# Kernel tuning notes

Hardware: AMD Instinct MI355X
Metric: run time of the kernel (lower is better)

The kernel has to match this reference:

```python
import jax, jax.numpy as jnp
import numpy as np

B, L, D = 32, 256, 128


def hard_sigmoid(x):
    # Keras-1 default inner_activation for LSTM gates
    return jnp.clip(0.2 * x + 0.5, 0.0, 1.0)


def lstm_step(x_t, h, c, W, U, b):
    # Keras-1 gate order: i, f, c(candidate), o
    z = x_t @ W + h @ U + b  # [B, 4D]
    d = h.shape[-1]
    i = hard_sigmoid(z[:, :d])
    f = hard_sigmoid(z[:, d:2 * d])
    g = jnp.tanh(z[:, 2 * d:3 * d])
    o = hard_sigmoid(z[:, 3 * d:])
    c_new = f * c + i * g
    h_new = o * jnp.tanh(c_new)
    return h_new, c_new


def setup_inputs() -> dict:
    key = jax.random.key(0)
    ks = jax.random.split(key, 9)
    s = 0.05  # weight scale to keep activations in a sane range
    return {
        "x": jax.random.normal(ks[0], (B, L, D), dtype=jnp.float32),
        "Wr": jax.random.normal(ks[1], (D, 4 * D), dtype=jnp.float32) * s,
        "Ur": jax.random.normal(ks[2], (D, 4 * D), dtype=jnp.float32) * s,
        "br": jnp.zeros((4 * D,), dtype=jnp.float32),
        "Ww": jax.random.normal(ks[3], (D, 4 * D), dtype=jnp.float32) * s,
        "Uw": jax.random.normal(ks[4], (D, 4 * D), dtype=jnp.float32) * s,
        "bw": jnp.zeros((4 * D,), dtype=jnp.float32),
        "Wc": jax.random.normal(ks[5], (2 * D, D), dtype=jnp.float32) * s,
        "bc": jnp.zeros((D,), dtype=jnp.float32),
    }


def reference(x, Wr, Ur, br, Ww, Uw, bw, Wc, bc):
    b, l, d = x.shape
    h0 = jnp.zeros((b, d), dtype=x.dtype)

    # ---- reader LSTM (return_sequences) ----
    def reader_step(carry, x_t):
        h, c = carry
        h, c = lstm_step(x_t, h, c, Wr, Ur, br)
        return (h, c), h

    _, o_seq = jax.lax.scan(reader_step, (h0, h0), jnp.swapaxes(x, 0, 1))  # [L, B, D]

    # ---- compose-and-write scan over timesteps ----
    mem0 = x  # read() sets mem_0 = input

    def write_step(carry, o_t):
        mem, h, c = carry  # mem: [B, L, D]
        # eq 2-3: attention over memory slots
        z = jax.nn.softmax(jnp.einsum('bd,bld->bl', o_t, mem), axis=-1)  # [B, L]
        m_rt = jnp.einsum('bl,bld->bd', z, mem)  # [B, D]
        # eq 4: composer (linear activation)
        c_t = jnp.concatenate([o_t, m_rt], axis=-1) @ Wc + bc  # [B, D]
        # eq 5: writer LSTM step
        h, c = lstm_step(c_t, h, c, Ww, Uw, bw)
        # eq 6: soft overwrite of memory
        zc = z[:, :, None]
        mem = mem * (1.0 - zc) + h[:, None, :] * zc
        return (mem, h, c), h

    (_, _, _), hs = jax.lax.scan(write_step, (mem0, h0, h0), o_seq)
    # return_mode == 'last_output'
    return hs[-1]
```

## Files before the change

kernel.cpp:

```cpp
#include <hip/hip_runtime.h>
#include <stdint.h>


#define LL 256

typedef float v2f __attribute__((ext_vector_type(2)));

__device__ __forceinline__ float hsig(float x) { return fminf(fmaxf(fmaf(x, 0.2f, 0.5f), 0.f), 1.f); }
__device__ __forceinline__ float tanh_fast(float x) {
  x = fminf(fmaxf(x, -15.f), 15.f);
  float e = __expf(2.f * x);
  return (e - 1.f) / (e + 1.f);
}

__global__ __launch_bounds__(512) void wtrans_kernel(const float* __restrict__ src,
                                                     float* __restrict__ dst, int jshift) {
  int idx = blockIdx.x * 512 + threadIdx.x;
  int J = 1 << jshift;
  int k = idx >> jshift, j = idx & (J - 1);
  dst[(((size_t)(k >> 2) << jshift) + j) * 4 + (k & 3)] = src[idx];
}

__global__ __launch_bounds__(512) void pvw_gemm(const float* __restrict__ Wc,
                                                const float* __restrict__ Ww,
                                                float* __restrict__ PVw) {
  __shared__ float wrow[128];
  const int r = blockIdx.x, j = threadIdx.x;
  if (j < 128) wrow[j] = Wc[r * 128 + j];
  __syncthreads();
  float a = 0.f;
#pragma unroll 4
  for (int m = 0; m < 128; m++) a = fmaf(wrow[m], Ww[m * 512 + j], a);
  PVw[r * 512 + j] = a;
}

__global__ __launch_bounds__(512) void pz_kernel(const float* __restrict__ bc,
                                                 const float* __restrict__ Ww,
                                                 const float* __restrict__ bw,
                                                 float* __restrict__ pz) {
  __shared__ float b_s[128];
  const int j = threadIdx.x;
  if (j < 128) b_s[j] = bc[j];
  __syncthreads();
  float a = bw[j];
#pragma unroll 4
  for (int m = 0; m < 128; m++) a = fmaf(b_s[m], Ww[m * 512 + j], a);
  pz[j] = a;
}

__global__ __launch_bounds__(512) void xw_gemm(const float* __restrict__ x,
                                               const float4* __restrict__ WrT4,
                                               const float* __restrict__ br,
                                               float* __restrict__ XW) {
  alignas(16) __shared__ float xs[8][128];
  const int b = blockIdx.x >> 5, tg = blockIdx.x & 31, tid = threadIdx.x;
  const float* xg = x + ((size_t)b * LL + tg * 8) * 128;
  if (tid < 256) ((float4*)&xs[0][0])[tid] = ((const float4*)xg)[tid];
  __syncthreads();
  float acc[8];
#pragma unroll
  for (int r = 0; r < 8; r++) acc[r] = 0.f;
#pragma unroll 8
  for (int i4 = 0; i4 < 32; i4++) {
    float4 w4 = WrT4[i4 * 512 + tid];
#pragma unroll
    for (int r = 0; r < 8; r++) {
      float4 v = *(const float4*)&xs[r][4 * i4];
      acc[r] += w4.x * v.x + w4.y * v.y + w4.z * v.z + w4.w * v.w;
    }
  }
  const float brj = br[tid];
  float* o = XW + ((size_t)b * LL + tg * 8) * 512;
#pragma unroll
  for (int r = 0; r < 8; r++) o[r * 512 + tid] = acc[r] + brj;
}

__global__ __launch_bounds__(512, 2) void reader_kernel(const float4* __restrict__ UrT4,
                                                        const float* __restrict__ XW,
                                                        float* __restrict__ og) {
  alignas(16) __shared__ float h_s[128];
  alignas(16) __shared__ float pp_s[512];
  const int b = blockIdx.x, tid = threadIdx.x;
  const float* XWb = XW + (size_t)b * LL * 512;
  float* ogb = og + (size_t)b * LL * 128;

  float4 U[32];
#pragma unroll
  for (int i4 = 0; i4 < 32; i4++) U[i4] = UrT4[i4 * 512 + tid];

  float c_r = 0.f;
  if (tid < 128) h_s[tid] = 0.f;
  float xwv = XWb[tid];
  __syncthreads();

  for (int t = 0; t < LL; t++) {
    float xw_n = (t + 1 < LL) ? XWb[(t + 1) * 512 + tid] : 0.f;
    v2f acc[4] = {{0.f, 0.f}, {0.f, 0.f}, {0.f, 0.f}, {0.f, 0.f}};
#pragma unroll
    for (int i4 = 0; i4 < 32; i4++) {
      float4 v = *(const float4*)&h_s[4 * i4];
      float4 w = U[i4];
      acc[i4 & 3] += (v2f){w.x, w.y} * (v2f){v.x, v.y};
      acc[i4 & 3] += (v2f){w.z, w.w} * (v2f){v.z, v.w};
    }
    v2f A = (acc[0] + acc[1]) + (acc[2] + acc[3]);
    pp_s[tid] = A.x + A.y + xwv;
    __syncthreads();
    if (tid < 128) {
      float zi = pp_s[tid], zf = pp_s[128 + tid], zg = pp_s[256 + tid], zo = pp_s[384 + tid];
      float ii = hsig(zi), ff = hsig(zf), gg = tanh_fast(zg), oo = hsig(zo);
      c_r = fmaf(ff, c_r, ii * gg);
      float h = oo * tanh_fast(c_r);
      h_s[tid] = h;
      ogb[t * 128 + tid] = h;
    }
    __syncthreads();
    xwv = xw_n;
  }
}

template <int NC>
__global__ __launch_bounds__(512, 2) void writer_kernel(
    const float* __restrict__ x,
    const float4* __restrict__ VwT4, const float4* __restrict__ UwT4,
    const float* __restrict__ og, const float* __restrict__ ZW,
    float* __restrict__ out) {
  alignas(16) __shared__ float h_s[128];
  alignas(16) __shared__ float osN[128];
  alignas(16) __shared__ float sc_s[256], ee_s[256];
  alignas(16) __shared__ float mr_s[128];
  alignas(16) __shared__ float pp_s[1024];
  __shared__ float rr_s[16];
  extern __shared__ float4 UwL[];

  const int b = blockIdx.x, tid = threadIdx.x;
  const int lane = tid & 63, wv = tid >> 6;
  const int l = tid >> 1, hf = tid & 1;
  const int q = tid >> 6, dp = tid & 63;

  const float* xg = x + (size_t)b * (LL * 128);
  const float* ogb = og + (size_t)b * (LL * 128);
  const float* ZWb = ZW + (size_t)b * (LL * 512);

  for (int i = tid; i < NC * 512; i += 512) UwL[i] = UwT4[i];

  float4 VR[16];
#pragma unroll
  for (int i4 = 0; i4 < 16; i4++) VR[i4] = VwT4[i4 * 512 + tid];

  v2f Mr[32], Mc[32];
#pragma unroll
  for (int w = 0; w < 32; w++) Mr[w] = *(const v2f*)(xg + l * 128 + hf * 64 + 2 * w);
#pragma unroll
  for (int i = 0; i < 32; i++) Mc[i] = *(const v2f*)(xg + (q * 32 + i) * 128 + 2 * dp);

  float c_w = 0.f;
  if (tid < 128) { h_s[tid] = 0.f; osN[tid] = ogb[tid]; }
  __syncthreads();
  {
    v2f S = {0.f, 0.f};
#pragma unroll
    for (int w = 0; w < 32; w++) S += Mr[w] * (*(const v2f*)&osN[hf * 64 + 2 * w]);
    float s = S.x + S.y;
    s += __shfl_xor(s, 1);
    if (hf == 0) sc_s[l] = s;
  }
  __syncthreads();

  for (int t = 0; t < LL; t++) {
    float huv;
    {
      float zwv = ZWb[(size_t)t * 512 + tid];
      v2f u0 = {0.f, 0.f}, u1 = {0.f, 0.f};
#pragma unroll 2
      for (int i4 = NC; i4 < 32; i4 += 2) {
        float4 w0 = UwT4[i4 * 512 + tid];
        float4 w1 = UwT4[(i4 + 1) * 512 + tid];
        float4 v0 = *(const float4*)&h_s[4 * i4];
        float4 v1 = *(const float4*)&h_s[4 * i4 + 4];
        u0 += (v2f){w0.x, w0.y} * (v2f){v0.x, v0.y};
        u0 += (v2f){w0.z, w0.w} * (v2f){v0.z, v0.w};
        u1 += (v2f){w1.x, w1.y} * (v2f){v1.x, v1.y};
        u1 += (v2f){w1.z, w1.w} * (v2f){v1.z, v1.w};
      }
#pragma unroll 2
      for (int i4 = 0; i4 < NC; i4 += 2) {
        float4 w0 = UwL[i4 * 512 + tid];
        float4 w1 = UwL[(i4 + 1) * 512 + tid];
        float4 v0 = *(const float4*)&h_s[4 * i4];
        float4 v1 = *(const float4*)&h_s[4 * i4 + 4];
        u0 += (v2f){w0.x, w0.y} * (v2f){v0.x, v0.y};
        u0 += (v2f){w0.z, w0.w} * (v2f){v0.z, v0.w};
        u1 += (v2f){w1.x, w1.y} * (v2f){v1.x, v1.y};
        u1 += (v2f){w1.z, w1.w} * (v2f){v1.z, v1.w};
      }
      v2f U = u0 + u1;
      huv = U.x + U.y + zwv;
    }
    if (tid >= 128 && tid < 256 && t + 1 < LL)
      osN[tid - 128] = ogb[(t + 1) * 128 + (tid - 128)];
    if (tid < 256) {
      float m = sc_s[tid];
#pragma unroll
      for (int off = 32; off > 0; off >>= 1) m = fmaxf(m, __shfl_xor(m, off));
      if (lane == 0) rr_s[wv] = m;
    }
    __syncthreads();
    if (tid < 256) {
      float mx = fmaxf(fmaxf(rr_s[0], rr_s[1]), fmaxf(rr_s[2], rr_s[3]));
      float e = __expf(sc_s[tid] - mx);
      ee_s[tid] = e;
      float s2 = e;
#pragma unroll
      for (int off = 32; off > 0; off >>= 1) s2 += __shfl_xor(s2, off);
      if (lane == 0) rr_s[8 + wv] = s2;
    }
    __syncthreads();
    const float inv = 1.f / (rr_s[8] + rr_s[9] + rr_s[10] + rr_s[11]);
    {
      v2f P = {0.f, 0.f};
#pragma unroll
      for (int i = 0; i < 32; i++) P += Mc[i] * ee_s[q * 32 + i];
      *(v2f*)&pp_s[q * 128 + 2 * dp] = P;
    }
    __syncthreads();
    if (tid < 128) {
      float s = 0.f;
#pragma unroll
      for (int g = 0; g < 8; g++) s += pp_s[g * 128 + tid];
      mr_s[tid] = s * inv;
    }
    __syncthreads();
    {
      v2f a0 = {0.f, 0.f}, a1 = {0.f, 0.f}, a2 = {0.f, 0.f}, a3 = {0.f, 0.f};
#pragma unroll 2
      for (int i4 = 16; i4 < 32; i4 += 2) {
        float4 w0 = VwT4[i4 * 512 + tid];
        float4 w1 = VwT4[(i4 + 1) * 512 + tid];
        float4 v0 = *(const float4*)&mr_s[4 * i4];
        float4 v1 = *(const float4*)&mr_s[4 * i4 + 4];
        a0 += (v2f){w0.x, w0.y} * (v2f){v0.x, v0.y};
        a0 += (v2f){w0.z, w0.w} * (v2f){v0.z, v0.w};
        a1 += (v2f){w1.x, w1.y} * (v2f){v1.x, v1.y};
        a1 += (v2f){w1.z, w1.w} * (v2f){v1.z, v1.w};
      }
#pragma unroll
      for (int i4 = 0; i4 < 16; i4 += 2) {
        float4 w0 = VR[i4];
        float4 w1 = VR[i4 + 1];
        float4 v0 = *(const float4*)&mr_s[4 * i4];
        float4 v1 = *(const float4*)&mr_s[4 * i4 + 4];
        a2 += (v2f){w0.x, w0.y} * (v2f){v0.x, v0.y};
        a2 += (v2f){w0.z, w0.w} * (v2f){v0.z, v0.w};
        a3 += (v2f){w1.x, w1.y} * (v2f){v1.x, v1.y};
        a3 += (v2f){w1.z, w1.w} * (v2f){v1.z, v1.w};
      }
      v2f A = (a0 + a2) + (a1 + a3);
      pp_s[tid] = A.x + A.y + huv;
    }
    __syncthreads();
    if (tid < 128) {
      float zi = pp_s[tid], zf = pp_s[128 + tid], zg = pp_s[256 + tid], zo = pp_s[384 + tid];
      float ii = hsig(zi), ff = hsig(zf), gg = tanh_fast(zg), oo = hsig(zo);
      c_w = fmaf(ff, c_w, ii * gg);
      h_s[tid] = oo * tanh_fast(c_w);
    }
    __syncthreads();
    if (t + 1 < LL) {
      const float zr = ee_s[l] * inv;
      v2f S = {0.f, 0.f};
#pragma unroll
      for (int w = 0; w < 32; w++) {
        v2f h2 = *(const v2f*)&h_s[hf * 64 + 2 * w];
        v2f m = Mr[w];
        v2f n = m + (h2 - m) * zr;
        Mr[w] = n;
        S += n * (*(const v2f*)&osN[hf * 64 + 2 * w]);
      }
      float s = S.x + S.y;
      s += __shfl_xor(s, 1);
      if (hf == 0) sc_s[l] = s;
      v2f hc = *(const v2f*)&h_s[2 * dp];
#pragma unroll
      for (int i = 0; i < 32; i++) {
        float zc = ee_s[q * 32 + i] * inv;
        v2f m = Mc[i];
        Mc[i] = m + (hc - m) * zc;
      }
    }
    __syncthreads();
  }

  if (tid < 128) out[b * 128 + tid] = h_s[tid];
}

extern "C" void kernel_launch(void* const* d_in, const int* in_sizes, int n_in,
                              void* d_out, int out_size, void* d_ws, size_t ws_size,
                              hipStream_t stream) {
  const float* x  = (const float*)d_in[0];
  const float* Wr = (const float*)d_in[1];
  const float* Ur = (const float*)d_in[2];
  const float* br = (const float*)d_in[3];
  const float* Ww = (const float*)d_in[4];
  const float* Uw = (const float*)d_in[5];
  const float* bw = (const float*)d_in[6];
  const float* Wc = (const float*)d_in[7];
  const float* bc = (const float*)d_in[8];
  float* out = (float*)d_out;

  float* og  = (float*)d_ws;
  float* XW  = og + 1048576;
  float* WrT = XW + 4194304;
  float* UrT = WrT + 65536;
  float* UwT = UrT + 65536;
  float* PVw = UwT + 65536;
  float* PwT = PVw + 131072;
  float* VwT = PwT + 65536;
  float* pz  = VwT + 65536;

  static int nc_cached = -1;
  if (nc_cached < 0) {
    int want = 18 * 512 * (int)sizeof(float4);
    nc_cached = (hipFuncSetAttribute(
                     reinterpret_cast<const void*>(&writer_kernel<18>),
                     hipFuncAttributeMaxDynamicSharedMemorySize, want) == hipSuccess)
                    ? 18
                    : 6;
  }

  wtrans_kernel<<<128, 512, 0, stream>>>(Wr, WrT, 9);
  wtrans_kernel<<<128, 512, 0, stream>>>(Ur, UrT, 9);
  wtrans_kernel<<<128, 512, 0, stream>>>(Uw, UwT, 9);
  pvw_gemm<<<256, 512, 0, stream>>>(Wc, Ww, PVw);
  pz_kernel<<<1, 512, 0, stream>>>(bc, Ww, bw, pz);
  wtrans_kernel<<<128, 512, 0, stream>>>(PVw, PwT, 9);
  wtrans_kernel<<<128, 512, 0, stream>>>(PVw + 65536, VwT, 9);
  xw_gemm<<<1024, 512, 0, stream>>>(x, (const float4*)WrT, br, XW);
  reader_kernel<<<32, 512, 0, stream>>>((const float4*)UrT, XW, og);
  xw_gemm<<<1024, 512, 0, stream>>>(og, (const float4*)PwT, pz, XW);
  if (nc_cached == 18) {
    writer_kernel<18><<<32, 512, 18 * 512 * sizeof(float4), stream>>>(
        x, (const float4*)VwT, (const float4*)UwT, og, XW, out);
  } else {
    writer_kernel<6><<<32, 512, 6 * 512 * sizeof(float4), stream>>>(
        x, (const float4*)VwT, (const float4*)UwT, og, XW, out);
  }
}
```

Measured before the change: 1.880 ms.

## Merge softmax reductions into one barrier, hold Uw slice in registers, prefetch ZW

The two-barrier softmax becomes a single pass. Each wave computes its local max and exp-sum, and the four wave partials are combined afterwards with rescaling factors. The 1/sum normalisation is folded into the Vw matvec output and the memory-update weights. The register-resident weight slice moves from 16 float4 of Vw to up to 14 float4 of Uw plus 4 of Vw, and the next step's ZW row is prefetched one iteration ahead. The intent is to remove a barrier and hide global-load latency, at the cost of register pressure under launch_bounds(512,2), with possible spills.

```diff
diff --git a/kernel.cpp b/kernel.cpp
--- a/kernel.cpp
+++ b/kernel.cpp
@@ -125,6 +125,9 @@
     const float4* __restrict__ VwT4, const float4* __restrict__ UwT4,
     const float* __restrict__ og, const float* __restrict__ ZW,
     float* __restrict__ out) {
+  constexpr int UR_N = (32 - NC < 14) ? (32 - NC) : 14;
+  constexpr int STR_LO = NC, STR_HI = 32 - UR_N;
+
   alignas(16) __shared__ float h_s[128];
   alignas(16) __shared__ float osN[128];
   alignas(16) __shared__ float sc_s[256], ee_s[256];
@@ -144,9 +147,13 @@
 
   for (int i = tid; i < NC * 512; i += 512) UwL[i] = UwT4[i];
 
-  float4 VR[16];
-#pragma unroll
-  for (int i4 = 0; i4 < 16; i4++) VR[i4] = VwT4[i4 * 512 + tid];
+  float4 UR[UR_N];
+#pragma unroll
+  for (int r = 0; r < UR_N; r++) UR[r] = UwT4[(size_t)(STR_HI + r) * 512 + tid];
+
+  float4 VR[4];
+#pragma unroll
+  for (int r = 0; r < 4; r++) VR[r] = VwT4[(size_t)(28 + r) * 512 + tid];
 
   v2f Mr[32], Mc[32];
 #pragma unroll
@@ -167,60 +174,70 @@
   }
   __syncthreads();
 
+  float zwv = ZWb[tid];
   for (int t = 0; t < LL; t++) {
+    const int tn = (t + 1 < LL) ? t + 1 : t;
+    float zw_n = ZWb[(size_t)tn * 512 + tid];
+
     float huv;
     {
-      float zwv = ZWb[(size_t)t * 512 + tid];
-      v2f u0 = {0.f, 0.f}, u1 = {0.f, 0.f};
+      v2f u0 = {0.f, 0.f}, u1 = {0.f, 0.f}, u2 = {0.f, 0.f}, u3 = {0.f, 0.f};
+#pragma unroll
+      for (int r = 0; r < UR_N; r++) {
+        float4 w = UR[r];
+        float4 v = *(const float4*)&h_s[4 * (STR_HI + r)];
+        u0 += (v2f){w.x, w.y} * (v2f){v.x, v.y};
+        u1 += (v2f){w.z, w.w} * (v2f){v.z, v.w};
+      }
 #pragma unroll 2
-      for (int i4 = NC; i4 < 32; i4 += 2) {
-        float4 w0 = UwT4[i4 * 512 + tid];
-        float4 w1 = UwT4[(i4 + 1) * 512 + tid];
-        float4 v0 = *(const float4*)&h_s[4 * i4];
-        float4 v1 = *(const float4*)&h_s[4 * i4 + 4];
-        u0 += (v2f){w0.x, w0.y} * (v2f){v0.x, v0.y};
-        u0 += (v2f){w0.z, w0.w} * (v2f){v0.z, v0.w};
-        u1 += (v2f){w1.x, w1.y} * (v2f){v1.x, v1.y};
-        u1 += (v2f){w1.z, w1.w} * (v2f){v1.z, v1.w};
+      for (int i4 = 0; i4 < NC; i4++) {
+        float4 w = UwL[i4 * 512 + tid];
+        float4 v = *(const float4*)&h_s[4 * i4];
+        u2 += (v2f){w.x, w.y} * (v2f){v.x, v.y};
+        u3 += (v2f){w.z, w.w} * (v2f){v.z, v.w};
       }
 #pragma unroll 2
-      for (int i4 = 0; i4 < NC; i4 += 2) {
-        float4 w0 = UwL[i4 * 512 + tid];
-        float4 w1 = UwL[(i4 + 1) * 512 + tid];
-        float4 v0 = *(const float4*)&h_s[4 * i4];
-        float4 v1 = *(const float4*)&h_s[4 * i4 + 4];
-        u0 += (v2f){w0.x, w0.y} * (v2f){v0.x, v0.y};
-        u0 += (v2f){w0.z, w0.w} * (v2f){v0.z, v0.w};
-        u1 += (v2f){w1.x, w1.y} * (v2f){v1.x, v1.y};
-        u1 += (v2f){w1.z, w1.w} * (v2f){v1.z, v1.w};
-      }
-      v2f U = u0 + u1;
+      for (int i4 = STR_LO; i4 < STR_HI; i4++) {
+        float4 w = UwT4[i4 * 512 + tid];
+        float4 v = *(const float4*)&h_s[4 * i4];
+        u2 += (v2f){w.x, w.y} * (v2f){v.x, v.y};
+        u3 += (v2f){w.z, w.w} * (v2f){v.z, v.w};
+      }
+      v2f U = (u0 + u1) + (u2 + u3);
       huv = U.x + U.y + zwv;
     }
+
     if (tid >= 128 && tid < 256 && t + 1 < LL)
       osN[tid - 128] = ogb[(t + 1) * 128 + (tid - 128)];
     if (tid < 256) {
-      float m = sc_s[tid];
+      float s = sc_s[tid];
+      float m = s;
 #pragma unroll
       for (int off = 32; off > 0; off >>= 1) m = fmaxf(m, __shfl_xor(m, off));
-      if (lane == 0) rr_s[wv] = m;
-    }
-    __syncthreads();
-    if (tid < 256) {
-      float mx = fmaxf(fmaxf(rr_s[0], rr_s[1]), fmaxf(rr_s[2], rr_s[3]));
-      float e = __expf(sc_s[tid] - mx);
+      float e = __expf(s - m);
       ee_s[tid] = e;
       float s2 = e;
 #pragma unroll
       for (int off = 32; off > 0; off >>= 1) s2 += __shfl_xor(s2, off);
-      if (lane == 0) rr_s[8 + wv] = s2;
-    }
-    __syncthreads();
-    const float inv = 1.f / (rr_s[8] + rr_s[9] + rr_s[10] + rr_s[11]);
+      if (lane == 0) { rr_s[wv] = m; rr_s[8 + wv] = s2; }
+    }
+    __syncthreads();
+
+    const float M = fmaxf(fmaxf(rr_s[0], rr_s[1]), fmaxf(rr_s[2], rr_s[3]));
+    const float Sg = rr_s[8] * __expf(rr_s[0] - M) + rr_s[9] * __expf(rr_s[1] - M) +
+                     rr_s[10] * __expf(rr_s[2] - M) + rr_s[11] * __expf(rr_s[3] - M);
+    const float inv = 1.f / Sg;
+    const float f = __expf(rr_s[tid >> 7] - M);
+    const float fzi = f * inv;
+
     {
-      v2f P = {0.f, 0.f};
-#pragma unroll
-      for (int i = 0; i < 32; i++) P += Mc[i] * ee_s[q * 32 + i];
+      v2f P0 = {0.f, 0.f}, P1 = {0.f, 0.f};
+#pragma unroll
+      for (int i = 0; i < 32; i += 2) {
+        P0 += Mc[i] * ee_s[q * 32 + i];
+        P1 += Mc[i + 1] * ee_s[q * 32 + i + 1];
+      }
+      v2f P = (P0 + P1) * f;
       *(v2f*)&pp_s[q * 128 + 2 * dp] = P;
     }
     __syncthreads();
@@ -228,13 +245,13 @@
       float s = 0.f;
 #pragma unroll
       for (int g = 0; g < 8; g++) s += pp_s[g * 128 + tid];
-      mr_s[tid] = s * inv;
+      mr_s[tid] = s;
     }
     __syncthreads();
     {
       v2f a0 = {0.f, 0.f}, a1 = {0.f, 0.f}, a2 = {0.f, 0.f}, a3 = {0.f, 0.f};
 #pragma unroll 2
-      for (int i4 = 16; i4 < 32; i4 += 2) {
+      for (int i4 = 0; i4 < 28; i4 += 2) {
         float4 w0 = VwT4[i4 * 512 + tid];
         float4 w1 = VwT4[(i4 + 1) * 512 + tid];
         float4 v0 = *(const float4*)&mr_s[4 * i4];
@@ -245,18 +262,14 @@
         a1 += (v2f){w1.z, w1.w} * (v2f){v1.z, v1.w};
       }
 #pragma unroll
-      for (int i4 = 0; i4 < 16; i4 += 2) {
-        float4 w0 = VR[i4];
-        float4 w1 = VR[i4 + 1];
-        float4 v0 = *(const float4*)&mr_s[4 * i4];
-        float4 v1 = *(const float4*)&mr_s[4 * i4 + 4];
-        a2 += (v2f){w0.x, w0.y} * (v2f){v0.x, v0.y};
-        a2 += (v2f){w0.z, w0.w} * (v2f){v0.z, v0.w};
-        a3 += (v2f){w1.x, w1.y} * (v2f){v1.x, v1.y};
-        a3 += (v2f){w1.z, w1.w} * (v2f){v1.z, v1.w};
+      for (int r = 0; r < 4; r++) {
+        float4 w = VR[r];
+        float4 v = *(const float4*)&mr_s[4 * (28 + r)];
+        a2 += (v2f){w.x, w.y} * (v2f){v.x, v.y};
+        a3 += (v2f){w.z, w.w} * (v2f){v.z, v.w};
       }
       v2f A = (a0 + a2) + (a1 + a3);
-      pp_s[tid] = A.x + A.y + huv;
+      pp_s[tid] = fmaf(A.x + A.y, inv, huv);
     }
     __syncthreads();
     if (tid < 128) {
@@ -267,28 +280,35 @@
     }
     __syncthreads();
     if (t + 1 < LL) {
-      const float zr = ee_s[l] * inv;
-      v2f S = {0.f, 0.f};
-#pragma unroll
-      for (int w = 0; w < 32; w++) {
-        v2f h2 = *(const v2f*)&h_s[hf * 64 + 2 * w];
-        v2f m = Mr[w];
-        v2f n = m + (h2 - m) * zr;
-        Mr[w] = n;
-        S += n * (*(const v2f*)&osN[hf * 64 + 2 * w]);
-      }
-      float s = S.x + S.y;
+      const float zr = ee_s[l] * fzi;
+      v2f S0v = {0.f, 0.f}, S1v = {0.f, 0.f};
+#pragma unroll
+      for (int w = 0; w < 32; w += 2) {
+        v2f h2a = *(const v2f*)&h_s[hf * 64 + 2 * w];
+        v2f ma = Mr[w];
+        v2f na = ma + (h2a - ma) * zr;
+        Mr[w] = na;
+        S0v += na * (*(const v2f*)&osN[hf * 64 + 2 * w]);
+        v2f h2b = *(const v2f*)&h_s[hf * 64 + 2 * (w + 1)];
+        v2f mb = Mr[w + 1];
+        v2f nb = mb + (h2b - mb) * zr;
+        Mr[w + 1] = nb;
+        S1v += nb * (*(const v2f*)&osN[hf * 64 + 2 * (w + 1)]);
+      }
+      v2f Sv = S0v + S1v;
+      float s = Sv.x + Sv.y;
       s += __shfl_xor(s, 1);
       if (hf == 0) sc_s[l] = s;
       v2f hc = *(const v2f*)&h_s[2 * dp];
 #pragma unroll
       for (int i = 0; i < 32; i++) {
-        float zc = ee_s[q * 32 + i] * inv;
+        float zc = ee_s[q * 32 + i] * fzi;
         v2f m = Mc[i];
         Mc[i] = m + (hc - m) * zc;
       }
     }
     __syncthreads();
+    zwv = zw_n;
   }
 
   if (tid < 128) out[b * 128 + tid] = h_s[tid];
```

New measurement: 2.829 ms. +50.4%, slower.
